# Performance work log

Measured on AMD Instinct MI355X. Metric: run time of the kernel, lower is better.

The kernel has to match this reference:

```python
import jax, jax.numpy as jnp
import numpy as np

N_EMBD = 2048
N_HEAD = 16
NUM_KV_GROUPS = 2
HEAD_DIM = N_EMBD // N_HEAD  # 128
GROUP_SIZE = N_HEAD // NUM_KV_GROUPS  # 8
EPS = 1e-8


def rmsnorm(x, gamma):
    rms = jnp.sqrt(jnp.mean(x * x, axis=-1, keepdims=True) + EPS)
    return x / rms * gamma


def setup_inputs() -> dict:
    key = jax.random.key(0)
    ks = jax.random.split(key, 10)
    s = 0.02
    x = jax.random.normal(ks[0], (2, 2048, N_EMBD), dtype=jnp.float32)
    Wq = jax.random.normal(ks[1], (N_EMBD, N_HEAD * HEAD_DIM), dtype=jnp.float32) * s
    bq = jnp.zeros((N_HEAD * HEAD_DIM,), jnp.float32)
    Wk = jax.random.normal(ks[2], (N_EMBD, NUM_KV_GROUPS * HEAD_DIM), dtype=jnp.float32) * s
    bk = jnp.zeros((NUM_KV_GROUPS * HEAD_DIM,), jnp.float32)
    Wv = jax.random.normal(ks[3], (N_EMBD, NUM_KV_GROUPS * HEAD_DIM), dtype=jnp.float32) * s
    bv = jnp.zeros((NUM_KV_GROUPS * HEAD_DIM,), jnp.float32)
    gamma_q = jnp.ones((HEAD_DIM,), jnp.float32)
    gamma_k = jnp.ones((HEAD_DIM,), jnp.float32)
    Wo = jax.random.normal(ks[4], (N_EMBD, N_EMBD), dtype=jnp.float32) * s
    bo = jnp.zeros((N_EMBD,), jnp.float32)
    return {"x": x, "Wq": Wq, "bq": bq, "Wk": Wk, "bk": bk, "Wv": Wv, "bv": bv,
            "gamma_q": gamma_q, "gamma_k": gamma_k, "Wo": Wo, "bo": bo}


def reference(x, Wq, bq, Wk, bk, Wv, bv, gamma_q, gamma_k, Wo, bo):
    B, S, E = x.shape
    # projections
    q = (x @ Wq + bq).reshape(B, S, N_HEAD, HEAD_DIM).transpose(0, 2, 1, 3)       # (B,H,S,D)
    k = (x @ Wk + bk).reshape(B, S, NUM_KV_GROUPS, HEAD_DIM).transpose(0, 2, 1, 3)  # (B,G,S,D)
    v = (x @ Wv + bv).reshape(B, S, NUM_KV_GROUPS, HEAD_DIM).transpose(0, 2, 1, 3)
    # fused per-head QK RMSNorm
    q = rmsnorm(q, gamma_q)
    k = rmsnorm(k, gamma_k)
    # GQA: broadcast each KV group to its GROUP_SIZE query heads (repeat_interleave on head dim)
    k = jnp.repeat(k, GROUP_SIZE, axis=1)  # (B,H,S,D)
    v = jnp.repeat(v, GROUP_SIZE, axis=1)
    scores = jnp.einsum('bhqd,bhkd->bhqk', q, k)
    causal = jnp.triu(jnp.ones((S, S), dtype=bool), k=1)
    scores = jnp.where(causal, -jnp.inf, scores)
    weights = jax.nn.softmax(scores / np.sqrt(HEAD_DIM).astype(np.float32), axis=-1)
    context = jnp.einsum('bhqk,bhkd->bhqd', weights, v)
    context = context.transpose(0, 2, 1, 3).reshape(B, S, E)
    return context @ Wo + bo
```

## Files before the change

kernel.cpp:

```cpp
#include <hip/hip_runtime.h>
#include <hip/hip_bf16.h>


typedef short  bf16x8 __attribute__((ext_vector_type(8)));
typedef float  f32x4  __attribute__((ext_vector_type(4)));
typedef unsigned short u16x8 __attribute__((ext_vector_type(8)));
typedef unsigned short u16x4 __attribute__((ext_vector_type(4)));

static __device__ __forceinline__ unsigned short f2bf(float f) {
    __hip_bfloat16 h = __float2bfloat16(f);
    return *reinterpret_cast<unsigned short*>(&h);
}

static __device__ __forceinline__ void load_lds16(const void* g, void* l) {
    __builtin_amdgcn_global_load_lds(
        (const __attribute__((address_space(1))) void*)g,
        (__attribute__((address_space(3))) void*)l, 16, 0, 0);
}

__global__ __launch_bounds__(256)
void cvt_bf16_k(const float* __restrict__ X, unsigned short* __restrict__ Y, int n8) {
    int i = blockIdx.x * 256 + threadIdx.x;
    if (i >= n8) return;
    float4 a = *(const float4*)(X + (size_t)i * 8);
    float4 b = *(const float4*)(X + (size_t)i * 8 + 4);
    u16x8 o{f2bf(a.x), f2bf(a.y), f2bf(a.z), f2bf(a.w),
            f2bf(b.x), f2bf(b.y), f2bf(b.z), f2bf(b.w)};
    *(u16x8*)(Y + (size_t)i * 8) = o;
}

__global__ __launch_bounds__(256)
void transpose_cvt2(const float* __restrict__ W, unsigned short* __restrict__ Wt,
                    int in_stride, int K) {
    __shared__ float t[32][33];
    int n0 = blockIdx.x * 32, k0 = blockIdx.y * 32;
    int tx = threadIdx.x & 31, ty = threadIdx.x >> 5;
#pragma unroll
    for (int i = 0; i < 32; i += 8)
        t[ty + i][tx] = W[(size_t)(k0 + ty + i) * in_stride + n0 + tx];
    __syncthreads();
#pragma unroll
    for (int i = 0; i < 32; i += 8)
        Wt[(size_t)(n0 + ty + i) * K + k0 + tx] = f2bf(t[tx][ty + i]);
}

__global__ __launch_bounds__(256)
void concat_bias(const float* __restrict__ bq, const float* __restrict__ bk,
                 const float* __restrict__ bv, float* __restrict__ o) {
    int i = blockIdx.x * 256 + threadIdx.x;
    if (i >= 2560) return;
    o[i] = (i < 2048) ? bq[i] : (i < 2304 ? bk[i - 2048] : bv[i - 2304]);
}

__global__ __launch_bounds__(256)
void gemm_lds(const unsigned short* __restrict__ A, const unsigned short* __restrict__ Bt,
              const float* __restrict__ bias, float* __restrict__ Cout,
              int M, int N, int K) {
    __shared__ unsigned short Al[2][128 * 32];
    __shared__ unsigned short Bl[2][128 * 32];
    int nwg = gridDim.x * gridDim.y;
    int bid = blockIdx.y * gridDim.x + blockIdx.x;
    int swz = (bid & 7) * (nwg >> 3) + (bid >> 3);
    int m0 = (swz / gridDim.x) * 128, n0 = (swz % gridDim.x) * 128;

    int tid = threadIdx.x, lane = tid & 63, w = tid >> 6;
    int wr = w >> 1, wc = w & 1, lg = lane >> 4, lr = lane & 15;

    f32x4 acc[4][4];
#pragma unroll
    for (int i = 0; i < 4; i++)
#pragma unroll
        for (int j = 0; j < 4; j++) acc[i][j] = f32x4{0.f, 0.f, 0.f, 0.f};

    int srow = w * 16 + (lane >> 2);
    int scol = (lane & 3) * 8;
    const unsigned short* ga = A  + (size_t)(m0 + srow) * K + scol;
    const unsigned short* gb = Bt + (size_t)(n0 + srow) * K + scol;

    auto stage = [&](int buf, int k0) {
        unsigned short* la = &Al[buf][w * 512];
        unsigned short* lb = &Bl[buf][w * 512];
        load_lds16(ga + k0,                  la);
        load_lds16(ga + (size_t)64 * K + k0, la + 2048);
        load_lds16(gb + k0,                  lb);
        load_lds16(gb + (size_t)64 * K + k0, lb + 2048);
    };
    stage(0, 0);
    __syncthreads();

    for (int k0 = 0; k0 < K; k0 += 32) {
        int cur = (k0 >> 5) & 1;
        if (k0 + 32 < K) stage(cur ^ 1, k0 + 32);
        bf16x8 af[4], bfv[4];
#pragma unroll
        for (int mi = 0; mi < 4; mi++)
            af[mi] = *(const bf16x8*)&Al[cur][(wr * 64 + mi * 16 + lr) * 32 + 8 * lg];
#pragma unroll
        for (int ni = 0; ni < 4; ni++)
            bfv[ni] = *(const bf16x8*)&Bl[cur][(wc * 64 + ni * 16 + lr) * 32 + 8 * lg];
#pragma unroll
        for (int mi = 0; mi < 4; mi++)
#pragma unroll
            for (int ni = 0; ni < 4; ni++)
                acc[mi][ni] = __builtin_amdgcn_mfma_f32_16x16x32_bf16(af[mi], bfv[ni], acc[mi][ni], 0, 0, 0);
        __syncthreads();
    }

#pragma unroll
    for (int mi = 0; mi < 4; mi++)
#pragma unroll
        for (int ni = 0; ni < 4; ni++) {
            int col = n0 + wc * 64 + ni * 16 + lr;
            float bv = bias[col];
#pragma unroll
            for (int r = 0; r < 4; r++) {
                int row = m0 + wr * 64 + mi * 16 + 4 * lg + r;
                Cout[(size_t)row * N + col] = acc[mi][ni][r] + bv;
            }
        }
}

__global__ __launch_bounds__(256)
void rmsnorm_cvt2(const float* __restrict__ C, const float* __restrict__ gamma,
                  unsigned short* __restrict__ Y, int in_stride, int in_off,
                  int cl, int total) {
    int wave = blockIdx.x * 4 + (threadIdx.x >> 6);
    int lane = threadIdx.x & 63;
    if (wave >= total) return;
    int token = wave >> cl, c = wave & ((1 << cl) - 1);
    const float* in = C + (size_t)token * in_stride + in_off + c * 128;
    float2 v = *(const float2*)(in + lane * 2);
    float ss = v.x * v.x + v.y * v.y;
#pragma unroll
    for (int m = 1; m < 64; m <<= 1) ss += __shfl_xor(ss, m);
    float inv = rsqrtf(ss * (1.0f / 128.0f) + 1e-8f);
    float2 gv = *(const float2*)(gamma + lane * 2);
    unsigned short o0 = f2bf(v.x * inv * gv.x);
    unsigned short o1 = f2bf(v.y * inv * gv.y);
    ((unsigned int*)Y)[((size_t)token * (1 << cl) + c) * 64 + lane] =
        (unsigned)o0 | ((unsigned)o1 << 16);
}

__global__ __launch_bounds__(256)
void attn_kernel(const unsigned short* __restrict__ Qb,
                 const unsigned short* __restrict__ Kb,
                 const unsigned short* __restrict__ Vt,
                 unsigned short* __restrict__ Ctx) {
    const int S = 2048;
    int pair = blockIdx.x, h = blockIdx.y, b = blockIdx.z, g = h >> 3;
    int tid = threadIdx.x, lane = tid & 63, w = tid >> 6;
    int lg = lane >> 4, lr = lane & 15;
    size_t tok0 = (size_t)b * S;

    __shared__ unsigned short Kl[2][64 * 128];
    __shared__ unsigned short Vl[2][128 * 64];
    __shared__ unsigned short Pl[4][16][72];

    const float cexp = 0.08838834764831845f * 1.4426950408889634f;

    int krow_l = w * 4 + (lane >> 4);
    int kc16   = (lane & 15) ^ (krow_l & 7);
    int vrow_l = w * 8 + (lane >> 3);
    int vc16   = (lane & 7) ^ (vrow_l & 7);
    const unsigned short* ksrcB = Kb + (tok0 + krow_l) * 256 + g * 128 + kc16 * 8;
    const unsigned short* vsrcB = Vt + (size_t)(g * 128 + vrow_l) * 4096 + b * S + vc16 * 8;
    int kswz = (lr & 7) << 3;

    auto stageKV = [&](int buf, int kvt) {
        const unsigned short* ks_ = ksrcB + (size_t)kvt * 64 * 256;
        unsigned short* kd = &Kl[buf][w * 512];
#pragma unroll
        for (int i = 0; i < 4; i++)
            load_lds16(ks_ + (size_t)i * 16 * 256, kd + i * 2048);
        const unsigned short* vs_ = vsrcB + kvt * 64;
        unsigned short* vd = &Vl[buf][w * 512];
#pragma unroll
        for (int i = 0; i < 4; i++)
            load_lds16(vs_ + (size_t)i * 32 * 4096, vd + i * 2048);
    };

    for (int hf = 0; hf < 2; hf++) {
        int qt = hf ? (31 - pair) : pair;
        int q0 = qt * 64 + w * 16;
        int myq = q0 + lr;

        bf16x8 qf[4];
#pragma unroll
        for (int ks = 0; ks < 4; ks++)
            qf[ks] = *(const bf16x8*)(Qb + (tok0 + myq) * 2048 + h * 128 + ks * 32 + 8 * lg);

        f32x4 o[8];
#pragma unroll
        for (int t = 0; t < 8; t++) o[t] = f32x4{0.f, 0.f, 0.f, 0.f};
        float mX = -1e30f, lX = 0.f;

        int nkv = qt + 1;
        stageKV(0, 0);
        __syncthreads();

        for (int kvt = 0; kvt < nkv; kvt++) {
            int cur = kvt & 1;
            int kv0 = kvt * 64;
            if (kvt + 1 < nkv) stageKV(cur ^ 1, kvt + 1);

            f32x4 sacc[4];
#pragma unroll
            for (int c = 0; c < 4; c++) sacc[c] = f32x4{0.f, 0.f, 0.f, 0.f};
#pragma unroll
            for (int c = 0; c < 4; c++) {
#pragma unroll
                for (int ks = 0; ks < 4; ks++) {
                    bf16x8 kf = *(const bf16x8*)&Kl[cur][(c * 16 + lr) * 128 + ((ks * 32 + 8 * lg) ^ kswz)];
                    sacc[c] = __builtin_amdgcn_mfma_f32_16x16x32_bf16(kf, qf[ks], sacc[c], 0, 0, 0);
                }
            }

            float pm = -1e30f;
            if (kvt == qt) {
#pragma unroll
                for (int c = 0; c < 4; c++)
#pragma unroll
                    for (int r = 0; r < 4; r++) {
                        float s = sacc[c][r] * cexp;
                        if (kv0 + c * 16 + 4 * lg + r > myq) s = -1e30f;
                        sacc[c][r] = s;
                        pm = fmaxf(pm, s);
                    }
            } else {
#pragma unroll
                for (int c = 0; c < 4; c++)
#pragma unroll
                    for (int r = 0; r < 4; r++) {
                        float s = sacc[c][r] * cexp;
                        sacc[c][r] = s;
                        pm = fmaxf(pm, s);
                    }
            }
            pm = fmaxf(pm, __shfl_xor(pm, 16));
            pm = fmaxf(pm, __shfl_xor(pm, 32));
            if (!__all(pm <= mX + 8.0f)) {
                float mn = fmaxf(mX, pm);
                float al = __builtin_exp2f(mX - mn);
                mX = mn;
                lX *= al;
#pragma unroll
                for (int t = 0; t < 8; t++)
#pragma unroll
                    for (int r = 0; r < 4; r++) o[t][r] *= al;
            }
            float ts = 0.f;
#pragma unroll
            for (int c = 0; c < 4; c++)
#pragma unroll
                for (int r = 0; r < 4; r++) {
                    float e = __builtin_exp2f(sacc[c][r] - mX);
                    sacc[c][r] = e;
                    ts += e;
                }
            ts += __shfl_xor(ts, 16);
            ts += __shfl_xor(ts, 32);
            lX += ts;

#pragma unroll
            for (int c = 0; c < 4; c++)
#pragma unroll
                for (int e = 0; e < 2; e++) {
                    unsigned u = (unsigned)f2bf(sacc[c][2 * e]) |
                                 ((unsigned)f2bf(sacc[c][2 * e + 1]) << 16);
                    *(unsigned*)&Pl[w][lr][c * 16 + 4 * lg + 2 * e] = u;
                }
            bf16x8 pf0 = *(const bf16x8*)&Pl[w][lr][8 * lg];
            bf16x8 pf1 = *(const bf16x8*)&Pl[w][lr][32 + 8 * lg];

#pragma unroll
            for (int t = 0; t < 8; t++) {
                bf16x8 vf0 = *(const bf16x8*)&Vl[cur][(t * 16 + lr) * 64 + ((8 * lg) ^ kswz)];
                bf16x8 vf1 = *(const bf16x8*)&Vl[cur][(t * 16 + lr) * 64 + ((32 + 8 * lg) ^ kswz)];
                o[t] = __builtin_amdgcn_mfma_f32_16x16x32_bf16(vf0, pf0, o[t], 0, 0, 0);
                o[t] = __builtin_amdgcn_mfma_f32_16x16x32_bf16(vf1, pf1, o[t], 0, 0, 0);
            }
            __syncthreads();
        }

        float inv = 1.0f / lX;
        unsigned short* crow = Ctx + (tok0 + myq) * 2048 + h * 128 + 4 * lg;
#pragma unroll
        for (int t = 0; t < 8; t++) {
            u16x4 pk{f2bf(o[t][0] * inv), f2bf(o[t][1] * inv),
                     f2bf(o[t][2] * inv), f2bf(o[t][3] * inv)};
            *(u16x4*)(crow + t * 16) = pk;
        }
    }
}

extern "C" void kernel_launch(void* const* d_in, const int* in_sizes, int n_in,
                              void* d_out, int out_size, void* d_ws, size_t ws_size,
                              hipStream_t stream) {
    const float* x  = (const float*)d_in[0];
    const float* Wq = (const float*)d_in[1];
    const float* bq = (const float*)d_in[2];
    const float* Wk = (const float*)d_in[3];
    const float* bk = (const float*)d_in[4];
    const float* Wv = (const float*)d_in[5];
    const float* bv = (const float*)d_in[6];
    const float* gq = (const float*)d_in[7];
    const float* gk = (const float*)d_in[8];
    const float* Wo = (const float*)d_in[9];
    const float* bo = (const float*)d_in[10];
    float* out = (float*)d_out;

    char* ws = (char*)d_ws;
    size_t off = 0;
    auto alloc = [&](size_t bytes) {
        void* p = ws + off;
        off += (bytes + 255) & ~(size_t)255;
        return p;
    };
    unsigned short* wqkvt = (unsigned short*)alloc((size_t)2560 * 2048 * 2);
    unsigned short* wot   = (unsigned short*)alloc((size_t)2048 * 2048 * 2);
    unsigned short* xb    = (unsigned short*)alloc((size_t)4096 * 2048 * 2);
    float*          C     = (float*)alloc((size_t)4096 * 2560 * 4);
    unsigned short* qb_   = (unsigned short*)alloc((size_t)4096 * 2048 * 2);
    unsigned short* kb_   = (unsigned short*)alloc((size_t)4096 * 256 * 2);
    unsigned short* vt    = (unsigned short*)alloc((size_t)512 * 4096 * 2);
    float*          biascat = (float*)alloc((size_t)2560 * 4);
    unsigned short* ctx = xb;

    cvt_bf16_k<<<4096, 256, 0, stream>>>(x, xb, 1048576);
    transpose_cvt2<<<dim3(64, 64), 256, 0, stream>>>(Wq, wqkvt, 2048, 2048);
    transpose_cvt2<<<dim3(8, 64),  256, 0, stream>>>(Wk, wqkvt + (size_t)2048 * 2048, 256, 2048);
    transpose_cvt2<<<dim3(8, 64),  256, 0, stream>>>(Wv, wqkvt + (size_t)2304 * 2048, 256, 2048);
    transpose_cvt2<<<dim3(64, 64), 256, 0, stream>>>(Wo, wot, 2048, 2048);
    concat_bias<<<10, 256, 0, stream>>>(bq, bk, bv, biascat);

    gemm_lds<<<dim3(20, 32), 256, 0, stream>>>(xb, wqkvt, biascat, C, 4096, 2560, 2048);

    rmsnorm_cvt2<<<16384, 256, 0, stream>>>(C, gq, qb_, 2560, 0,    4, 65536);
    rmsnorm_cvt2<<<2048,  256, 0, stream>>>(C, gk, kb_, 2560, 2048, 1, 8192);
    transpose_cvt2<<<dim3(16, 128), 256, 0, stream>>>(C + 2304, vt, 2560, 4096);

    attn_kernel<<<dim3(16, 16, 2), 256, 0, stream>>>(qb_, kb_, vt, ctx);

    gemm_lds<<<dim3(16, 32), 256, 0, stream>>>(ctx, wot, bo, out, 4096, 2048, 2048);
}
```

Measured before the change: 327.0 us.

## Process both paired query tiles in one KV sweep to share K/V loads

The attention kernel used to handle its two query tiles (pair and 31-pair) one after the other, streaming K/V twice. It now walks the KV range once for the longer tile and reuses each staged K/V tile for both query tiles, computing the short tile only while kvt <= qtA. This halves K/V global-to-LDS traffic and the barrier count, and gives more independent MFMA work per LDS fragment read. In exchange it doubles the live accumulator registers, which may cut occupancy. It also XOR-swizzles the P scratch buffer to avoid bank conflicts.

```diff
diff --git a/kernel.cpp b/kernel.cpp
--- a/kernel.cpp
+++ b/kernel.cpp
@@ -154,7 +154,7 @@
 
     __shared__ unsigned short Kl[2][64 * 128];
     __shared__ unsigned short Vl[2][128 * 64];
-    __shared__ unsigned short Pl[4][16][72];
+    __shared__ unsigned short Pl[4][2][16][64];
 
     const float cexp = 0.08838834764831845f * 1.4426950408889634f;
 
@@ -166,131 +166,147 @@
     const unsigned short* vsrcB = Vt + (size_t)(g * 128 + vrow_l) * 4096 + b * S + vc16 * 8;
     int kswz = (lr & 7) << 3;
 
-    auto stageKV = [&](int buf, int kvt) {
-        const unsigned short* ks_ = ksrcB + (size_t)kvt * 64 * 256;
-        unsigned short* kd = &Kl[buf][w * 512];
-#pragma unroll
-        for (int i = 0; i < 4; i++)
-            load_lds16(ks_ + (size_t)i * 16 * 256, kd + i * 2048);
-        const unsigned short* vs_ = vsrcB + kvt * 64;
-        unsigned short* vd = &Vl[buf][w * 512];
-#pragma unroll
-        for (int i = 0; i < 4; i++)
-            load_lds16(vs_ + (size_t)i * 32 * 4096, vd + i * 2048);
-    };
-
-    for (int hf = 0; hf < 2; hf++) {
-        int qt = hf ? (31 - pair) : pair;
-        int q0 = qt * 64 + w * 16;
-        int myq = q0 + lr;
-
-        bf16x8 qf[4];
-#pragma unroll
-        for (int ks = 0; ks < 4; ks++)
-            qf[ks] = *(const bf16x8*)(Qb + (tok0 + myq) * 2048 + h * 128 + ks * 32 + 8 * lg);
-
-        f32x4 o[8];
-#pragma unroll
-        for (int t = 0; t < 8; t++) o[t] = f32x4{0.f, 0.f, 0.f, 0.f};
-        float mX = -1e30f, lX = 0.f;
-
-        int nkv = qt + 1;
-        stageKV(0, 0);
+#define STAGE_KV(buf, kvt_) {                                                    \
+    const unsigned short* ks_ = ksrcB + (size_t)(kvt_) * 64 * 256;               \
+    unsigned short* kd = &Kl[buf][w * 512];                                      \
+    _Pragma("unroll")                                                            \
+    for (int i = 0; i < 4; i++)                                                  \
+        load_lds16(ks_ + (size_t)i * 16 * 256, kd + i * 2048);                   \
+    const unsigned short* vs_ = vsrcB + (kvt_) * 64;                             \
+    unsigned short* vd = &Vl[buf][w * 512];                                      \
+    _Pragma("unroll")                                                            \
+    for (int i = 0; i < 4; i++)                                                  \
+        load_lds16(vs_ + (size_t)i * 32 * 4096, vd + i * 2048);                  \
+}
+
+    int qtA = pair, qtB = 31 - pair;
+    int qA = qtA * 64 + w * 16 + lr;
+    int qB = qtB * 64 + w * 16 + lr;
+
+    bf16x8 qfA[4], qfB[4];
+#pragma unroll
+    for (int ks = 0; ks < 4; ks++) {
+        qfA[ks] = *(const bf16x8*)(Qb + (tok0 + qA) * 2048 + h * 128 + ks * 32 + 8 * lg);
+        qfB[ks] = *(const bf16x8*)(Qb + (tok0 + qB) * 2048 + h * 128 + ks * 32 + 8 * lg);
+    }
+
+    f32x4 oA[8], oB[8];
+#pragma unroll
+    for (int t = 0; t < 8; t++) { oA[t] = f32x4{0.f,0.f,0.f,0.f}; oB[t] = f32x4{0.f,0.f,0.f,0.f}; }
+    float mA = -1e30f, lA = 0.f, mB = -1e30f, lB = 0.f;
+
+#define SOFTMAX_STEP(sacc, mX, lX, oX, myq, isdiag, slot) {                      \
+    float pm = -1e30f;                                                           \
+    _Pragma("unroll")                                                            \
+    for (int c = 0; c < 4; c++)                                                  \
+        _Pragma("unroll")                                                        \
+        for (int r = 0; r < 4; r++) {                                            \
+            float s = sacc[c][r] * cexp;                                         \
+            if (isdiag && (kv0 + c * 16 + 4 * lg + r > myq)) s = -1e30f;         \
+            sacc[c][r] = s;                                                      \
+            pm = fmaxf(pm, s);                                                   \
+        }                                                                        \
+    pm = fmaxf(pm, __shfl_xor(pm, 16));                                          \
+    pm = fmaxf(pm, __shfl_xor(pm, 32));                                          \
+    if (!__all(pm <= mX + 8.0f)) {                                               \
+        float mn = fmaxf(mX, pm);                                                \
+        float al = __builtin_exp2f(mX - mn);                                     \
+        mX = mn;                                                                 \
+        lX *= al;                                                                \
+        _Pragma("unroll")                                                        \
+        for (int t = 0; t < 8; t++)                                              \
+            _Pragma("unroll")                                                    \
+            for (int r = 0; r < 4; r++) oX[t][r] *= al;                          \
+    }                                                                            \
+    float ts = 0.f;                                                              \
+    _Pragma("unroll")                                                            \
+    for (int c = 0; c < 4; c++)                                                  \
+        _Pragma("unroll")                                                        \
+        for (int r = 0; r < 4; r++) {                                            \
+            float e = __builtin_exp2f(sacc[c][r] - mX);                          \
+            sacc[c][r] = e;                                                      \
+            ts += e;                                                             \
+        }                                                                        \
+    ts += __shfl_xor(ts, 16);                                                    \
+    ts += __shfl_xor(ts, 32);                                                    \
+    lX += ts;                                                                    \
+    _Pragma("unroll")                                                            \
+    for (int c = 0; c < 4; c++)                                                  \
+        _Pragma("unroll")                                                        \
+        for (int e = 0; e < 2; e++) {                                            \
+            unsigned u = (unsigned)f2bf(sacc[c][2 * e]) |                        \
+                         ((unsigned)f2bf(sacc[c][2 * e + 1]) << 16);             \
+            *(unsigned*)&Pl[w][slot][lr][(16 * c + 4 * lg + 2 * e) ^ kswz] = u;  \
+        }                                                                        \
+}
+
+    int nkv = qtB + 1;
+    STAGE_KV(0, 0);
+    __syncthreads();
+
+    for (int kvt = 0; kvt < nkv; kvt++) {
+        int cur = kvt & 1;
+        int kv0 = kvt * 64;
+        if (kvt + 1 < nkv) STAGE_KV(cur ^ 1, kvt + 1);
+        bool doA = (kvt <= qtA);
+
+        f32x4 sA[4], sB[4];
+#pragma unroll
+        for (int c = 0; c < 4; c++) { sA[c] = f32x4{0.f,0.f,0.f,0.f}; sB[c] = f32x4{0.f,0.f,0.f,0.f}; }
+#pragma unroll
+        for (int c = 0; c < 4; c++) {
+            bf16x8 kf[4];
+#pragma unroll
+            for (int ks = 0; ks < 4; ks++)
+                kf[ks] = *(const bf16x8*)&Kl[cur][(c * 16 + lr) * 128 + ((ks * 32 + 8 * lg) ^ kswz)];
+#pragma unroll
+            for (int ks = 0; ks < 4; ks++) {
+                sB[c] = __builtin_amdgcn_mfma_f32_16x16x32_bf16(kf[ks], qfB[ks], sB[c], 0, 0, 0);
+                if (doA)
+                    sA[c] = __builtin_amdgcn_mfma_f32_16x16x32_bf16(kf[ks], qfA[ks], sA[c], 0, 0, 0);
+            }
+        }
+
+        SOFTMAX_STEP(sB, mB, lB, oB, qB, (kvt == qtB), 0);
+        if (doA) SOFTMAX_STEP(sA, mA, lA, oA, qA, (kvt == qtA), 1);
+
+        bf16x8 pB0 = *(const bf16x8*)&Pl[w][0][lr][(8 * lg) ^ kswz];
+        bf16x8 pB1 = *(const bf16x8*)&Pl[w][0][lr][(32 + 8 * lg) ^ kswz];
+        bf16x8 pA0, pA1;
+        if (doA) {
+            pA0 = *(const bf16x8*)&Pl[w][1][lr][(8 * lg) ^ kswz];
+            pA1 = *(const bf16x8*)&Pl[w][1][lr][(32 + 8 * lg) ^ kswz];
+        }
+
+#pragma unroll
+        for (int t = 0; t < 8; t++) {
+            bf16x8 vf0 = *(const bf16x8*)&Vl[cur][(t * 16 + lr) * 64 + ((8 * lg) ^ kswz)];
+            bf16x8 vf1 = *(const bf16x8*)&Vl[cur][(t * 16 + lr) * 64 + ((32 + 8 * lg) ^ kswz)];
+            oB[t] = __builtin_amdgcn_mfma_f32_16x16x32_bf16(vf0, pB0, oB[t], 0, 0, 0);
+            oB[t] = __builtin_amdgcn_mfma_f32_16x16x32_bf16(vf1, pB1, oB[t], 0, 0, 0);
+            if (doA) {
+                oA[t] = __builtin_amdgcn_mfma_f32_16x16x32_bf16(vf0, pA0, oA[t], 0, 0, 0);
+                oA[t] = __builtin_amdgcn_mfma_f32_16x16x32_bf16(vf1, pA1, oA[t], 0, 0, 0);
+            }
+        }
         __syncthreads();
-
-        for (int kvt = 0; kvt < nkv; kvt++) {
-            int cur = kvt & 1;
-            int kv0 = kvt * 64;
-            if (kvt + 1 < nkv) stageKV(cur ^ 1, kvt + 1);
-
-            f32x4 sacc[4];
-#pragma unroll
-            for (int c = 0; c < 4; c++) sacc[c] = f32x4{0.f, 0.f, 0.f, 0.f};
-#pragma unroll
-            for (int c = 0; c < 4; c++) {
-#pragma unroll
-                for (int ks = 0; ks < 4; ks++) {
-                    bf16x8 kf = *(const bf16x8*)&Kl[cur][(c * 16 + lr) * 128 + ((ks * 32 + 8 * lg) ^ kswz)];
-                    sacc[c] = __builtin_amdgcn_mfma_f32_16x16x32_bf16(kf, qf[ks], sacc[c], 0, 0, 0);
-                }
-            }
-
-            float pm = -1e30f;
-            if (kvt == qt) {
-#pragma unroll
-                for (int c = 0; c < 4; c++)
-#pragma unroll
-                    for (int r = 0; r < 4; r++) {
-                        float s = sacc[c][r] * cexp;
-                        if (kv0 + c * 16 + 4 * lg + r > myq) s = -1e30f;
-                        sacc[c][r] = s;
-                        pm = fmaxf(pm, s);
-                    }
-            } else {
-#pragma unroll
-                for (int c = 0; c < 4; c++)
-#pragma unroll
-                    for (int r = 0; r < 4; r++) {
-                        float s = sacc[c][r] * cexp;
-                        sacc[c][r] = s;
-                        pm = fmaxf(pm, s);
-                    }
-            }
-            pm = fmaxf(pm, __shfl_xor(pm, 16));
-            pm = fmaxf(pm, __shfl_xor(pm, 32));
-            if (!__all(pm <= mX + 8.0f)) {
-                float mn = fmaxf(mX, pm);
-                float al = __builtin_exp2f(mX - mn);
-                mX = mn;
-                lX *= al;
-#pragma unroll
-                for (int t = 0; t < 8; t++)
-#pragma unroll
-                    for (int r = 0; r < 4; r++) o[t][r] *= al;
-            }
-            float ts = 0.f;
-#pragma unroll
-            for (int c = 0; c < 4; c++)
-#pragma unroll
-                for (int r = 0; r < 4; r++) {
-                    float e = __builtin_exp2f(sacc[c][r] - mX);
-                    sacc[c][r] = e;
-                    ts += e;
-                }
-            ts += __shfl_xor(ts, 16);
-            ts += __shfl_xor(ts, 32);
-            lX += ts;
-
-#pragma unroll
-            for (int c = 0; c < 4; c++)
-#pragma unroll
-                for (int e = 0; e < 2; e++) {
-                    unsigned u = (unsigned)f2bf(sacc[c][2 * e]) |
-                                 ((unsigned)f2bf(sacc[c][2 * e + 1]) << 16);
-                    *(unsigned*)&Pl[w][lr][c * 16 + 4 * lg + 2 * e] = u;
-                }
-            bf16x8 pf0 = *(const bf16x8*)&Pl[w][lr][8 * lg];
-            bf16x8 pf1 = *(const bf16x8*)&Pl[w][lr][32 + 8 * lg];
-
-#pragma unroll
-            for (int t = 0; t < 8; t++) {
-                bf16x8 vf0 = *(const bf16x8*)&Vl[cur][(t * 16 + lr) * 64 + ((8 * lg) ^ kswz)];
-                bf16x8 vf1 = *(const bf16x8*)&Vl[cur][(t * 16 + lr) * 64 + ((32 + 8 * lg) ^ kswz)];
-                o[t] = __builtin_amdgcn_mfma_f32_16x16x32_bf16(vf0, pf0, o[t], 0, 0, 0);
-                o[t] = __builtin_amdgcn_mfma_f32_16x16x32_bf16(vf1, pf1, o[t], 0, 0, 0);
-            }
-            __syncthreads();
-        }
-
-        float inv = 1.0f / lX;
-        unsigned short* crow = Ctx + (tok0 + myq) * 2048 + h * 128 + 4 * lg;
-#pragma unroll
-        for (int t = 0; t < 8; t++) {
-            u16x4 pk{f2bf(o[t][0] * inv), f2bf(o[t][1] * inv),
-                     f2bf(o[t][2] * inv), f2bf(o[t][3] * inv)};
-            *(u16x4*)(crow + t * 16) = pk;
-        }
     }
+
+#define EPILOGUE(oX, lX, myq) {                                                  \
+    float inv = 1.0f / lX;                                                       \
+    unsigned short* crow = Ctx + (tok0 + myq) * 2048 + h * 128 + 4 * lg;         \
+    _Pragma("unroll")                                                            \
+    for (int t = 0; t < 8; t++) {                                                \
+        u16x4 pk{f2bf(oX[t][0] * inv), f2bf(oX[t][1] * inv),                     \
+                 f2bf(oX[t][2] * inv), f2bf(oX[t][3] * inv)};                    \
+        *(u16x4*)(crow + t * 16) = pk;                                           \
+    }                                                                            \
+}
+    EPILOGUE(oB, lB, qB);
+    EPILOGUE(oA, lA, qA);
+#undef STAGE_KV
+#undef SOFTMAX_STEP
+#undef EPILOGUE
 }
 
 extern "C" void kernel_launch(void* const* d_in, const int* in_sizes, int n_in,
```

New measurement: 408.4 us. 1.25x slower.
